# Kernel tuning notes

Hardware: AMD Instinct MI355X
Metric: run time of the kernel (lower is better)

## Reference

```python
import jax, jax.numpy as jnp
import numpy as np
from jax import lax

R = 2048          # proposals per image
K = 20            # foreground classes (VOC)
IMG_H, IMG_W = 800, 1333   # image_shape (height, width)
SCORE_THRESH = 0.5
NMS_THRESH = 0.5
TOPK = 100


def setup_inputs() -> dict:
    key = jax.random.key(0)
    k1, k2, k3 = jax.random.split(key, 3)
    # well-formed xyxy boxes roughly inside the image (some spill past edges to exercise clipping)
    xy = jax.random.uniform(k1, (R, 2)) * jnp.array([IMG_W * 0.9, IMG_H * 0.9], jnp.float32)
    wh = jax.random.uniform(k2, (R, 2)) * jnp.array([IMG_W * 0.3, IMG_H * 0.3], jnp.float32) + 4.0
    boxes = jnp.concatenate([xy, xy + wh], axis=1).astype(jnp.float32)          # [R,4]
    scores = jax.random.uniform(k3, (R, K + 1), dtype=jnp.float32)              # [R,K+1]
    return {"boxes": boxes, "scores": scores}


def _pairwise_iou(b):
    # b: [R,4] xyxy -> [R,R] IoU
    area = (b[:, 2] - b[:, 0]) * (b[:, 3] - b[:, 1])
    lt = jnp.maximum(b[:, None, :2], b[None, :, :2])
    rb = jnp.minimum(b[:, None, 2:], b[None, :, 2:])
    wh = jnp.clip(rb - lt, 0.0)
    inter = wh[..., 0] * wh[..., 1]
    union = area[:, None] + area[None, :] - inter
    return inter / jnp.maximum(union, 1e-9)


def _nms_single_class(scores_c, valid_c, boxes):
    # Greedy NMS over one class; padded candidates carry valid=False and never
    # get kept nor suppress anything (matches torchvision nms semantics).
    order = jnp.argsort(-scores_c)                      # descending by score
    iou = _pairwise_iou(boxes[order])                   # [R,R]
    v = valid_c[order]
    idx = jnp.arange(R)

    def body(i, keep):
        suppressed = jnp.any(keep & (iou[i] > NMS_THRESH) & (idx < i))
        return keep.at[i].set(v[i] & ~suppressed)

    keep_sorted = lax.fori_loop(0, R, body, jnp.zeros((R,), bool))
    return jnp.zeros((R,), bool).at[order].set(keep_sorted)


def reference(boxes, scores):
    scores_fg = scores[:, :-1]                                            # drop background col -> [R,K]
    finite = jnp.all(jnp.isfinite(boxes), axis=1) & jnp.all(jnp.isfinite(scores), axis=1)
    # Boxes.clip(image_shape): x in [0,W], y in [0,H]
    bx = jnp.stack([jnp.clip(boxes[:, 0], 0.0, IMG_W),
                    jnp.clip(boxes[:, 1], 0.0, IMG_H),
                    jnp.clip(boxes[:, 2], 0.0, IMG_W),
                    jnp.clip(boxes[:, 3], 0.0, IMG_H)], axis=1)           # [R,4]
    filt = (scores_fg > SCORE_THRESH) & finite[:, None]                    # [R,K]
    # batched_nms: independent greedy NMS per class (vmapped over classes)
    keep = jax.vmap(_nms_single_class, in_axes=(1, 1, None))(scores_fg, filt, bx)  # [K,R]
    masked = jnp.where(keep, scores_fg.T, -jnp.inf).reshape(-1)            # [K*R]
    top_s, top_i = lax.top_k(masked, TOPK)                                 # global topk (= keep[:topk])
    pred_classes = top_i // R
    pred_inds = top_i % R
    top_b = bx[pred_inds]                                                  # [TOPK,4]
    return top_s, top_b, pred_classes, pred_inds
```

## Files before the change

### kernel.cpp

```cpp
#include <hip/hip_runtime.h>
#include <hip/hip_bf16.h>
#include <math.h>

#define R 2048
#define K 20
#define TOPK 100
#define SCORE_TH 0.5f
#define NMS_TH 0.5f
#define IMGW 1333.0f
#define IMGH 800.0f

typedef unsigned long long u64;
typedef unsigned int u32;

#define MAPF_MINF 0x007FFFFFu
#define MAPF_TH 0xBF000000u

__device__ __forceinline__ u32 mapf(float f) {
  u32 b = __float_as_uint(f);
  return (b & 0x80000000u) ? ~b : (b | 0x80000000u);
}
__device__ __forceinline__ float unmapf(u32 u) {
  u32 b = (u & 0x80000000u) ? (u & 0x7FFFFFFFu) : ~u;
  return __uint_as_float(b);
}

__global__ void prep_kernel(const float* __restrict__ boxes,
                            const float* __restrict__ scores,
                            float* __restrict__ bx,
                            int* __restrict__ finite) {
  int r = blockIdx.x * blockDim.x + threadIdx.x;
  if (r >= R) return;
  float x1 = boxes[r * 4 + 0], y1 = boxes[r * 4 + 1];
  float x2 = boxes[r * 4 + 2], y2 = boxes[r * 4 + 3];
  bool fin = isfinite(x1) && isfinite(y1) && isfinite(x2) && isfinite(y2);
  for (int c = 0; c < K + 1; ++c) fin = fin && isfinite(scores[r * (K + 1) + c]);
  bx[r * 4 + 0] = fminf(fmaxf(x1, 0.0f), IMGW);
  bx[r * 4 + 1] = fminf(fmaxf(y1, 0.0f), IMGH);
  bx[r * 4 + 2] = fminf(fmaxf(x2, 0.0f), IMGW);
  bx[r * 4 + 3] = fminf(fmaxf(y2, 0.0f), IMGH);
  finite[r] = fin ? 1 : 0;
}

__global__ __launch_bounds__(1024) void sort_kernel(const float* __restrict__ scores,
                                                    const float* __restrict__ bx,
                                                    const int* __restrict__ finite,
                                                    u64* __restrict__ sortedkey,
                                                    float4* __restrict__ sboxs,
                                                    int* __restrict__ nvalid) {
  const int c = blockIdx.x;
  const int tid = threadIdx.x;
  __shared__ u64 sk[R];
  for (int r = tid; r < R; r += 1024) {
    float s = scores[r * (K + 1) + c];
    bool valid = (s > SCORE_TH) && (finite[r] != 0);
    u32 hi = valid ? mapf(s) : MAPF_MINF;
    sk[r] = ((u64)hi << 32) | (u32)(~(u32)r);
  }
  __syncthreads();
  for (int k = 2; k <= R; k <<= 1) {
    for (int j = k >> 1; j > 0; j >>= 1) {
      for (int i = tid; i < R; i += 1024) {
        int ixj = i ^ j;
        if (ixj > i) {
          u64 a = sk[i], b = sk[ixj];
          bool sw = ((i & k) == 0) ? (a < b) : (a > b);
          if (sw) { sk[i] = b; sk[ixj] = a; }
        }
      }
      __syncthreads();
    }
  }
  u64* skg = sortedkey + (size_t)c * R;
  float4* sbg = sboxs + (size_t)c * R;
  for (int i = tid; i < R; i += 1024) {
    u64 key = sk[i];
    skg[i] = key;
    u32 r = ~(u32)key;
    sbg[i] = reinterpret_cast<const float4*>(bx)[r];
    bool vi = ((u32)(key >> 32)) > MAPF_TH;
    if (i == 0 && !vi) nvalid[c] = 0;
    if (vi) {
      bool vlast = (i == R - 1);
      bool vn = vlast ? false : (((u32)(sk[i + 1] >> 32)) > MAPF_TH);
      if (vlast || !vn) nvalid[c] = i + 1;
    }
  }
}

__global__ __launch_bounds__(1024) void mask_kernel(const float4* __restrict__ sboxs,
                                                    const int* __restrict__ nvalid,
                                                    u64* __restrict__ maskbuf) {
  const int c = blockIdx.x;
  const int tid = threadIdx.x;
  const int lane = tid & 63;
  const int wave = tid >> 6;
  __shared__ float4 sb[R];
  __shared__ float sa[R];
  const float4* sbg = sboxs + (size_t)c * R;
  const int nv = nvalid[c];
  for (int i = tid; i < R; i += 1024) {
    float4 b = sbg[i];
    sb[i] = b;
    sa[i] = (b.z - b.x) * (b.w - b.y);
  }
  __syncthreads();
  const int wend = (nv + 63) >> 6;
  u64* mrowbase = maskbuf + (size_t)c * R * 32;
  for (int row = blockIdx.y * 16 + wave; row < nv; row += 128) {
    float4 b = sb[row];
    float ai = sa[row];
    u64 myword = 0;
    int wstart = row >> 6;
    for (int w = wstart; w < wend; ++w) {
      int col = (w << 6) + lane;
      float4 q = sb[col];
      float lx = fmaxf(b.x, q.x), ly = fmaxf(b.y, q.y);
      float rx = fminf(b.z, q.z), ry = fminf(b.w, q.w);
      float ww = fmaxf(rx - lx, 0.0f), hh = fmaxf(ry - ly, 0.0f);
      float inter = ww * hh;
      float uni = ai + sa[col] - inter;
      bool bit = (col > row) && (inter / fmaxf(uni, 1e-9f) > NMS_TH);
      u64 word = __ballot(bit);
      if (lane == w) myword = word;
    }
    u64* mrow = mrowbase + (size_t)row * 32;
    if (lane < 32) mrow[lane] = myword;
  }
}

__global__ __launch_bounds__(64) void scan_kernel(const u64* __restrict__ sortedkey,
                                                  const int* __restrict__ nvalid,
                                                  const u64* __restrict__ maskbuf,
                                                  u64* __restrict__ keybuf) {
  const int c = blockIdx.x;
  const int lane = threadIdx.x;
  const int nv = nvalid[c];
  const u64* mb = maskbuf + (size_t)c * R * 32;
  u64 remv = 0, keepm = 0;
  u64 ring[16];
#pragma unroll
  for (int s = 0; s < 16; ++s)
    ring[s] = (s < nv && lane < 32) ? mb[(size_t)s * 32 + lane] : 0ULL;
  for (int ib = 0; ib < nv; ib += 16) {
#pragma unroll
    for (int s = 0; s < 16; ++s) {
      int i = ib + s;
      bool act = i < nv;
      int widx = i >> 6;
      int bit = i & 63;
      u64 wv = __shfl(remv, widx, 64);
      bool keep = act && !((wv >> bit) & 1ULL);
      if (keep) {
        remv |= ring[s];
        if (lane == widx) keepm |= (1ULL << bit);
      }
      int ipf = i + 16;
      ring[s] = (ipf < nv && lane < 32) ? mb[(size_t)ipf * 32 + lane] : 0ULL;
    }
  }
  __shared__ u64 kw[32];
  if (lane < 32) kw[lane] = keepm;
  __syncthreads();
  const u64* skg = sortedkey + (size_t)c * R;
  for (int i = lane; i < R; i += 64) {
    u64 key = skg[i];
    bool kept = (i < nv) && ((kw[i >> 6] >> (i & 63)) & 1ULL);
    u32 r = ~(u32)key;
    u32 flat = (u32)c * R + r;
    u32 hi = kept ? (u32)(key >> 32) : MAPF_MINF;
    keybuf[flat] = ((u64)hi << 32) | (u32)(~flat);
  }
}

__global__ __launch_bounds__(64) void nms_kernel(const float* __restrict__ scores,
                                                 const float* __restrict__ bx,
                                                 const int* __restrict__ finite,
                                                 u64* __restrict__ keybuf) {
  const int c = blockIdx.x;
  const int lane = threadIdx.x;
  __shared__ u64 skeys[R];
  __shared__ float4 sbox[R];
  __shared__ float sarea[R];
  __shared__ unsigned short kidx[R];
  __shared__ unsigned char keepr[R];
  for (int r = lane; r < R; r += 64) {
    float s = scores[r * (K + 1) + c];
    bool valid = (s > SCORE_TH) && (finite[r] != 0);
    float sv = valid ? s : -INFINITY;
    skeys[r] = ((u64)mapf(sv) << 32) | (u32)(~(u32)r);
    keepr[r] = 0;
  }
  __syncthreads();
  for (int k = 2; k <= R; k <<= 1) {
    for (int j = k >> 1; j > 0; j >>= 1) {
      for (int i = lane; i < R; i += 64) {
        int ixj = i ^ j;
        if (ixj > i) {
          u64 a = skeys[i], b = skeys[ixj];
          bool sw = ((i & k) == 0) ? (a < b) : (a > b);
          if (sw) { skeys[i] = b; skeys[ixj] = a; }
        }
      }
      __syncthreads();
    }
  }
  for (int i = lane; i < R; i += 64) {
    int r = (int)(~(u32)skeys[i]);
    const float4 b = reinterpret_cast<const float4*>(bx)[r];
    sbox[i] = b;
    sarea[i] = (b.z - b.x) * (b.w - b.y);
  }
  __syncthreads();
  int m = 0;
  for (int i = 0; i < R; ++i) {
    u64 key = skeys[i];
    float s = unmapf((u32)(key >> 32));
    if (!(s > SCORE_TH)) break;
    int r = (int)(~(u32)key);
    float4 b = sbox[i];
    float ai = sarea[i];
    bool sup = false;
    for (int j = lane; j < m; j += 64) {
      int jj = kidx[j];
      float4 kb = sbox[jj];
      float lx = fmaxf(b.x, kb.x), ly = fmaxf(b.y, kb.y);
      float rx = fminf(b.z, kb.z), ry = fminf(b.w, kb.w);
      float w = fmaxf(rx - lx, 0.0f), h = fmaxf(ry - ly, 0.0f);
      float inter = w * h;
      float uni = ai + sarea[jj] - inter;
      if (inter / fmaxf(uni, 1e-9f) > NMS_TH) sup = true;
    }
    bool kept = !__any(sup);
    if (kept) {
      if (lane == 0) { kidx[m] = (unsigned short)i; keepr[r] = 1; }
      __syncthreads();
      m++;
    }
  }
  __syncthreads();
  for (int r = lane; r < R; r += 64) {
    float s = scores[r * (K + 1) + c];
    u32 flat = (u32)(c * R + r);
    float sv = keepr[r] ? s : -INFINITY;
    keybuf[flat] = ((u64)mapf(sv) << 32) | (u32)(~flat);
  }
}

__global__ __launch_bounds__(1024) void chunk_kernel(const u64* __restrict__ in,
                                                     int nin,
                                                     u64* __restrict__ outk) {
  const int t = blockIdx.x;
  const int tid = threadIdx.x;
  __shared__ u64 s[1024];
  int gi = t * 1024 + tid;
  s[tid] = (gi < nin) ? in[gi] : 0ULL;
  __syncthreads();
  for (int k = 2; k <= 1024; k <<= 1) {
    for (int j = k >> 1; j > 0; j >>= 1) {
      int ixj = tid ^ j;
      if (ixj > tid) {
        u64 a = s[tid], b = s[ixj];
        bool sw = ((tid & k) == 0) ? (a < b) : (a > b);
        if (sw) { s[tid] = b; s[ixj] = a; }
      }
      __syncthreads();
    }
  }
  if (tid < 128) outk[t * 128 + tid] = s[tid];
}

__global__ __launch_bounds__(1024) void final_kernel(const u64* __restrict__ cand,
                                                     int nin,
                                                     const float* __restrict__ bx,
                                                     float* __restrict__ out) {
  const int tid = threadIdx.x;
  __shared__ u64 s[1024];
  s[tid] = (tid < nin) ? cand[tid] : 0ULL;
  __syncthreads();
  for (int k = 2; k <= 1024; k <<= 1) {
    for (int j = k >> 1; j > 0; j >>= 1) {
      int ixj = tid ^ j;
      if (ixj > tid) {
        u64 a = s[tid], b = s[ixj];
        bool sw = ((tid & k) == 0) ? (a < b) : (a > b);
        if (sw) { s[tid] = b; s[ixj] = a; }
      }
      __syncthreads();
    }
  }
  if (tid < TOPK) {
    u64 key = s[tid];
    float sc = unmapf((u32)(key >> 32));
    u32 flat = ~(u32)key;
    int c = (int)(flat >> 11);
    int r = (int)(flat & 2047);
    out[tid] = sc;
    out[100 + 4 * tid + 0] = bx[r * 4 + 0];
    out[100 + 4 * tid + 1] = bx[r * 4 + 1];
    out[100 + 4 * tid + 2] = bx[r * 4 + 2];
    out[100 + 4 * tid + 3] = bx[r * 4 + 3];
    out[500 + tid] = (float)c;
    out[600 + tid] = (float)r;
  }
}

extern "C" void kernel_launch(void* const* d_in, const int* in_sizes, int n_in,
                              void* d_out, int out_size, void* d_ws, size_t ws_size,
                              hipStream_t stream) {
  const float* boxes = (const float*)d_in[0];
  const float* scores = (const float*)d_in[1];
  float* out = (float*)d_out;
  char* ws = (char*)d_ws;
  float* bx = (float*)(ws + 0);
  int* finite = (int*)(ws + 32768);
  (void)in_sizes; (void)n_in; (void)out_size;

  prep_kernel<<<8, 256, 0, stream>>>(boxes, scores, bx, finite);

  if (ws_size >= 11908096) {
    u64* sortedkey = (u64*)(ws + 40960);
    float4* sboxs = (float4*)(ws + 368640);
    int* nvalid = (int*)(ws + 1024000);
    u64* maskbuf = (u64*)(ws + 1048576);
    u64* keybuf = (u64*)(ws + 11534336);
    u64* cand1 = (u64*)(ws + 11862016);
    u64* cand2 = (u64*)(ws + 11902976);
    sort_kernel<<<K, 1024, 0, stream>>>(scores, bx, finite, sortedkey, sboxs, nvalid);
    mask_kernel<<<dim3(K, 8), 1024, 0, stream>>>(sboxs, nvalid, maskbuf);
    scan_kernel<<<K, 64, 0, stream>>>(sortedkey, nvalid, maskbuf, keybuf);
    chunk_kernel<<<40, 1024, 0, stream>>>(keybuf, K * R, cand1);
    chunk_kernel<<<5, 1024, 0, stream>>>(cand1, 5120, cand2);
    final_kernel<<<1, 1024, 0, stream>>>(cand2, 640, bx, out);
  } else {
    u64* keybuf = (u64*)(ws + 40960);
    u64* cand1 = (u64*)(ws + 368640);
    u64* cand2 = (u64*)(ws + 409600);
    nms_kernel<<<K, 64, 0, stream>>>(scores, bx, finite, keybuf);
    chunk_kernel<<<40, 1024, 0, stream>>>(keybuf, K * R, cand1);
    chunk_kernel<<<5, 1024, 0, stream>>>(cand1, 5120, cand2);
    final_kernel<<<1, 1024, 0, stream>>>(cand2, 640, bx, out);
  }
}
```

Measured before the change: 257.2 us.

## Fuse prep into sort, stage mask rows in LDS, emit per-class top-128 candidates

Folds the box clipping and finiteness check into the per-class sort kernel, which removes the prep launch and its intermediate buffers. The scan kernel now double-buffers 64-row mask windows in shared memory and compacts kept detections into at most 128 candidates per class plus a keep bitmap. A single final kernel sorts the 2560 candidates and fills any tail slots with -inf entries, replacing two chunk-sort launches. The fallback nms path is dropped, and each class sort now rereads all score columns per row to test finiteness.

```diff
diff --git a/kernel.cpp b/kernel.cpp
--- a/kernel.cpp
+++ b/kernel.cpp
@@ -24,36 +24,35 @@
   u32 b = (u & 0x80000000u) ? (u & 0x7FFFFFFFu) : ~u;
   return __uint_as_float(b);
 }
-
-__global__ void prep_kernel(const float* __restrict__ boxes,
-                            const float* __restrict__ scores,
-                            float* __restrict__ bx,
-                            int* __restrict__ finite) {
-  int r = blockIdx.x * blockDim.x + threadIdx.x;
-  if (r >= R) return;
-  float x1 = boxes[r * 4 + 0], y1 = boxes[r * 4 + 1];
-  float x2 = boxes[r * 4 + 2], y2 = boxes[r * 4 + 3];
-  bool fin = isfinite(x1) && isfinite(y1) && isfinite(x2) && isfinite(y2);
-  for (int c = 0; c < K + 1; ++c) fin = fin && isfinite(scores[r * (K + 1) + c]);
-  bx[r * 4 + 0] = fminf(fmaxf(x1, 0.0f), IMGW);
-  bx[r * 4 + 1] = fminf(fmaxf(y1, 0.0f), IMGH);
-  bx[r * 4 + 2] = fminf(fmaxf(x2, 0.0f), IMGW);
-  bx[r * 4 + 3] = fminf(fmaxf(y2, 0.0f), IMGH);
-  finite[r] = fin ? 1 : 0;
+__device__ __forceinline__ float4 clipbox(float4 b) {
+  float4 o;
+  o.x = fminf(fmaxf(b.x, 0.0f), IMGW);
+  o.y = fminf(fmaxf(b.y, 0.0f), IMGH);
+  o.z = fminf(fmaxf(b.z, 0.0f), IMGW);
+  o.w = fminf(fmaxf(b.w, 0.0f), IMGH);
+  return o;
 }
 
 __global__ __launch_bounds__(1024) void sort_kernel(const float* __restrict__ scores,
-                                                    const float* __restrict__ bx,
-                                                    const int* __restrict__ finite,
+                                                    const float* __restrict__ boxes,
                                                     u64* __restrict__ sortedkey,
                                                     float4* __restrict__ sboxs,
                                                     int* __restrict__ nvalid) {
   const int c = blockIdx.x;
   const int tid = threadIdx.x;
   __shared__ u64 sk[R];
+  __shared__ float4 cb[R];
   for (int r = tid; r < R; r += 1024) {
-    float s = scores[r * (K + 1) + c];
-    bool valid = (s > SCORE_TH) && (finite[r] != 0);
+    float4 b = reinterpret_cast<const float4*>(boxes)[r];
+    bool fin = isfinite(b.x) && isfinite(b.y) && isfinite(b.z) && isfinite(b.w);
+    float s = 0.0f;
+    for (int c2 = 0; c2 < K + 1; ++c2) {
+      float v = scores[r * (K + 1) + c2];
+      fin = fin && isfinite(v);
+      if (c2 == c) s = v;
+    }
+    cb[r] = clipbox(b);
+    bool valid = (s > SCORE_TH) && fin;
     u32 hi = valid ? mapf(s) : MAPF_MINF;
     sk[r] = ((u64)hi << 32) | (u32)(~(u32)r);
   }
@@ -76,8 +75,8 @@
   for (int i = tid; i < R; i += 1024) {
     u64 key = sk[i];
     skg[i] = key;
-    u32 r = ~(u32)key;
-    sbg[i] = reinterpret_cast<const float4*>(bx)[r];
+    u32 r = (~(u32)key) & 2047u;
+    sbg[i] = cb[r];
     bool vi = ((u32)(key >> 32)) > MAPF_TH;
     if (i == 0 && !vi) nvalid[c] = 0;
     if (vi) {
@@ -132,176 +131,156 @@
 __global__ __launch_bounds__(64) void scan_kernel(const u64* __restrict__ sortedkey,
                                                   const int* __restrict__ nvalid,
                                                   const u64* __restrict__ maskbuf,
-                                                  u64* __restrict__ keybuf) {
+                                                  u64* __restrict__ cand,
+                                                  int* __restrict__ nkept,
+                                                  u32* __restrict__ keepbm) {
   const int c = blockIdx.x;
   const int lane = threadIdx.x;
   const int nv = nvalid[c];
   const u64* mb = maskbuf + (size_t)c * R * 32;
+  const u64* skg = sortedkey + (size_t)c * R;
+  __shared__ u64 win[2][2048];
+  __shared__ u64 keepw[32];
+  __shared__ int pref[32];
+  __shared__ u64 lcand[128];
+  __shared__ u32 bm[64];
+  if (lane < 32) keepw[lane] = 0;
+  bm[lane] = 0;
+  lcand[lane] = 0;
+  lcand[lane + 64] = 0;
+
+  const int ngroups = (nv + 63) >> 6;
+  if (ngroups > 0) {
+    int lim = (nv < 64 ? nv : 64) * 32;
+    for (int t = lane; t < 2048; t += 64) win[0][t] = (t < lim) ? mb[t] : 0;
+  }
+  __syncthreads();
+
   u64 remv = 0, keepm = 0;
-  u64 ring[16];
-#pragma unroll
-  for (int s = 0; s < 16; ++s)
-    ring[s] = (s < nv && lane < 32) ? mb[(size_t)s * 32 + lane] : 0ULL;
-  for (int ib = 0; ib < nv; ib += 16) {
-#pragma unroll
-    for (int s = 0; s < 16; ++s) {
-      int i = ib + s;
-      bool act = i < nv;
-      int widx = i >> 6;
-      int bit = i & 63;
-      u64 wv = __shfl(remv, widx, 64);
-      bool keep = act && !((wv >> bit) & 1ULL);
+  for (int g = 0; g < ngroups; ++g) {
+    const int buf = g & 1;
+    if (g + 1 < ngroups) {
+      int base = (g + 1) << 6;
+      int nrows = nv - base; if (nrows > 64) nrows = 64;
+      int lim = nrows * 32;
+      for (int t = lane; t < 2048; t += 64)
+        win[buf ^ 1][t] = (t < lim) ? mb[(size_t)base * 32 + t] : 0;
+    }
+    const int rb = g << 6;
+    int rend = nv - rb; if (rend > 64) rend = 64;
+    for (int b = 0; b < rend; ++b) {
+      u64 wv = __shfl(remv, g, 64);
+      bool keep = !((wv >> b) & 1ull);
       if (keep) {
-        remv |= ring[s];
-        if (lane == widx) keepm |= (1ULL << bit);
+        u64 v = (lane < 32) ? win[buf][b * 32 + lane] : 0;
+        remv |= v;
+        if (lane == g) keepm |= (1ull << b);
       }
-      int ipf = i + 16;
-      ring[s] = (ipf < nv && lane < 32) ? mb[(size_t)ipf * 32 + lane] : 0ULL;
-    }
-  }
-  __shared__ u64 kw[32];
-  if (lane < 32) kw[lane] = keepm;
-  __syncthreads();
-  const u64* skg = sortedkey + (size_t)c * R;
-  for (int i = lane; i < R; i += 64) {
-    u64 key = skg[i];
-    bool kept = (i < nv) && ((kw[i >> 6] >> (i & 63)) & 1ULL);
-    u32 r = ~(u32)key;
-    u32 flat = (u32)c * R + r;
-    u32 hi = kept ? (u32)(key >> 32) : MAPF_MINF;
-    keybuf[flat] = ((u64)hi << 32) | (u32)(~flat);
-  }
-}
-
-__global__ __launch_bounds__(64) void nms_kernel(const float* __restrict__ scores,
-                                                 const float* __restrict__ bx,
-                                                 const int* __restrict__ finite,
-                                                 u64* __restrict__ keybuf) {
-  const int c = blockIdx.x;
-  const int lane = threadIdx.x;
-  __shared__ u64 skeys[R];
-  __shared__ float4 sbox[R];
-  __shared__ float sarea[R];
-  __shared__ unsigned short kidx[R];
-  __shared__ unsigned char keepr[R];
-  for (int r = lane; r < R; r += 64) {
-    float s = scores[r * (K + 1) + c];
-    bool valid = (s > SCORE_TH) && (finite[r] != 0);
-    float sv = valid ? s : -INFINITY;
-    skeys[r] = ((u64)mapf(sv) << 32) | (u32)(~(u32)r);
-    keepr[r] = 0;
-  }
-  __syncthreads();
-  for (int k = 2; k <= R; k <<= 1) {
+    }
+    __syncthreads();
+  }
+  if (lane < 32) keepw[lane] = keepm;
+  __syncthreads();
+  if (lane == 0) {
+    int run = 0;
+    for (int g = 0; g < ngroups; ++g) { pref[g] = run; run += (int)__popcll(keepw[g]); }
+    nkept[c] = run;
+  }
+  __syncthreads();
+  for (int g = 0; g < ngroups; ++g) {
+    u64 kw = keepw[g];
+    if ((kw >> lane) & 1ull) {
+      u64 below = lane ? (kw & ((1ull << lane) - 1ull)) : 0ull;
+      int slot = pref[g] + (int)__popcll(below);
+      u64 key = skg[(g << 6) + lane];
+      u32 r = (~(u32)key) & 2047u;
+      u32 flat = (u32)c * R + r;
+      atomicOr(&bm[r >> 5], 1u << (r & 31));
+      if (slot < 128) lcand[slot] = (key & 0xFFFFFFFF00000000ull) | (u64)(u32)(~flat);
+    }
+  }
+  __syncthreads();
+  cand[(size_t)c * 128 + lane] = lcand[lane];
+  cand[(size_t)c * 128 + 64 + lane] = lcand[lane + 64];
+  keepbm[c * 64 + lane] = bm[lane];
+}
+
+__global__ __launch_bounds__(1024) void final_kernel(const u64* __restrict__ cand,
+                                                     const int* __restrict__ nkept,
+                                                     const u32* __restrict__ keepbm,
+                                                     const float* __restrict__ boxes,
+                                                     float* __restrict__ out) {
+  const int tid = threadIdx.x;
+  __shared__ u64 s[4096];
+  __shared__ int nk_sh;
+  for (int i = tid; i < 4096; i += 1024) s[i] = (i < K * 128) ? cand[i] : 0ULL;
+  if (tid == 0) {
+    int nk = 0;
+    for (int c = 0; c < K; ++c) nk += nkept[c];
+    nk_sh = nk;
+  }
+  __syncthreads();
+  for (int k = 2; k <= 4096; k <<= 1) {
     for (int j = k >> 1; j > 0; j >>= 1) {
-      for (int i = lane; i < R; i += 64) {
+      for (int i = tid; i < 4096; i += 1024) {
         int ixj = i ^ j;
         if (ixj > i) {
-          u64 a = skeys[i], b = skeys[ixj];
+          u64 a = s[i], b = s[ixj];
           bool sw = ((i & k) == 0) ? (a < b) : (a > b);
-          if (sw) { skeys[i] = b; skeys[ixj] = a; }
+          if (sw) { s[i] = b; s[ixj] = a; }
         }
       }
       __syncthreads();
     }
   }
-  for (int i = lane; i < R; i += 64) {
-    int r = (int)(~(u32)skeys[i]);
-    const float4 b = reinterpret_cast<const float4*>(bx)[r];
-    sbox[i] = b;
-    sarea[i] = (b.z - b.x) * (b.w - b.y);
-  }
-  __syncthreads();
-  int m = 0;
-  for (int i = 0; i < R; ++i) {
-    u64 key = skeys[i];
-    float s = unmapf((u32)(key >> 32));
-    if (!(s > SCORE_TH)) break;
-    int r = (int)(~(u32)key);
-    float4 b = sbox[i];
-    float ai = sarea[i];
-    bool sup = false;
-    for (int j = lane; j < m; j += 64) {
-      int jj = kidx[j];
-      float4 kb = sbox[jj];
-      float lx = fmaxf(b.x, kb.x), ly = fmaxf(b.y, kb.y);
-      float rx = fminf(b.z, kb.z), ry = fminf(b.w, kb.w);
-      float w = fmaxf(rx - lx, 0.0f), h = fmaxf(ry - ly, 0.0f);
-      float inter = w * h;
-      float uni = ai + sarea[jj] - inter;
-      if (inter / fmaxf(uni, 1e-9f) > NMS_TH) sup = true;
-    }
-    bool kept = !__any(sup);
-    if (kept) {
-      if (lane == 0) { kidx[m] = (unsigned short)i; keepr[r] = 1; }
-      __syncthreads();
-      m++;
-    }
-  }
-  __syncthreads();
-  for (int r = lane; r < R; r += 64) {
-    float s = scores[r * (K + 1) + c];
-    u32 flat = (u32)(c * R + r);
-    float sv = keepr[r] ? s : -INFINITY;
-    keybuf[flat] = ((u64)mapf(sv) << 32) | (u32)(~flat);
-  }
-}
-
-__global__ __launch_bounds__(1024) void chunk_kernel(const u64* __restrict__ in,
-                                                     int nin,
-                                                     u64* __restrict__ outk) {
-  const int t = blockIdx.x;
-  const int tid = threadIdx.x;
-  __shared__ u64 s[1024];
-  int gi = t * 1024 + tid;
-  s[tid] = (gi < nin) ? in[gi] : 0ULL;
-  __syncthreads();
-  for (int k = 2; k <= 1024; k <<= 1) {
-    for (int j = k >> 1; j > 0; j >>= 1) {
-      int ixj = tid ^ j;
-      if (ixj > tid) {
-        u64 a = s[tid], b = s[ixj];
-        bool sw = ((tid & k) == 0) ? (a < b) : (a > b);
-        if (sw) { s[tid] = b; s[ixj] = a; }
+  const int nk = nk_sh;
+  if (nk >= TOPK) {
+    if (tid < TOPK) {
+      u64 key = s[tid];
+      u32 flat = ~(u32)key;
+      int c = (int)(flat >> 11);
+      int r = (int)(flat & 2047);
+      float4 b = clipbox(reinterpret_cast<const float4*>(boxes)[r]);
+      out[tid] = unmapf((u32)(key >> 32));
+      out[100 + 4 * tid + 0] = b.x;
+      out[100 + 4 * tid + 1] = b.y;
+      out[100 + 4 * tid + 2] = b.z;
+      out[100 + 4 * tid + 3] = b.w;
+      out[500 + tid] = (float)c;
+      out[600 + tid] = (float)r;
+    }
+  } else {
+    if (tid < nk) {
+      u64 key = s[tid];
+      u32 flat = ~(u32)key;
+      int c = (int)(flat >> 11);
+      int r = (int)(flat & 2047);
+      float4 b = clipbox(reinterpret_cast<const float4*>(boxes)[r]);
+      out[tid] = unmapf((u32)(key >> 32));
+      out[100 + 4 * tid + 0] = b.x;
+      out[100 + 4 * tid + 1] = b.y;
+      out[100 + 4 * tid + 2] = b.z;
+      out[100 + 4 * tid + 3] = b.w;
+      out[500 + tid] = (float)c;
+      out[600 + tid] = (float)r;
+    }
+    if (tid == 0) {
+      int w = nk;
+      for (u32 f = 0; f < (u32)(K * R) && w < TOPK; ++f) {
+        u32 cc = f >> 11, rr = f & 2047u;
+        if (!((keepbm[cc * 64 + (rr >> 5)] >> (rr & 31)) & 1u)) {
+          float4 b = clipbox(reinterpret_cast<const float4*>(boxes)[rr]);
+          out[w] = -INFINITY;
+          out[100 + 4 * w + 0] = b.x;
+          out[100 + 4 * w + 1] = b.y;
+          out[100 + 4 * w + 2] = b.z;
+          out[100 + 4 * w + 3] = b.w;
+          out[500 + w] = (float)cc;
+          out[600 + w] = (float)rr;
+          ++w;
+        }
       }
-      __syncthreads();
-    }
-  }
-  if (tid < 128) outk[t * 128 + tid] = s[tid];
-}
-
-__global__ __launch_bounds__(1024) void final_kernel(const u64* __restrict__ cand,
-                                                     int nin,
-                                                     const float* __restrict__ bx,
-                                                     float* __restrict__ out) {
-  const int tid = threadIdx.x;
-  __shared__ u64 s[1024];
-  s[tid] = (tid < nin) ? cand[tid] : 0ULL;
-  __syncthreads();
-  for (int k = 2; k <= 1024; k <<= 1) {
-    for (int j = k >> 1; j > 0; j >>= 1) {
-      int ixj = tid ^ j;
-      if (ixj > tid) {
-        u64 a = s[tid], b = s[ixj];
-        bool sw = ((tid & k) == 0) ? (a < b) : (a > b);
-        if (sw) { s[tid] = b; s[ixj] = a; }
-      }
-      __syncthreads();
-    }
-  }
-  if (tid < TOPK) {
-    u64 key = s[tid];
-    float sc = unmapf((u32)(key >> 32));
-    u32 flat = ~(u32)key;
-    int c = (int)(flat >> 11);
-    int r = (int)(flat & 2047);
-    out[tid] = sc;
-    out[100 + 4 * tid + 0] = bx[r * 4 + 0];
-    out[100 + 4 * tid + 1] = bx[r * 4 + 1];
-    out[100 + 4 * tid + 2] = bx[r * 4 + 2];
-    out[100 + 4 * tid + 3] = bx[r * 4 + 3];
-    out[500 + tid] = (float)c;
-    out[600 + tid] = (float)r;
+    }
   }
 }
 
@@ -312,33 +291,17 @@
   const float* scores = (const float*)d_in[1];
   float* out = (float*)d_out;
   char* ws = (char*)d_ws;
-  float* bx = (float*)(ws + 0);
-  int* finite = (int*)(ws + 32768);
-  (void)in_sizes; (void)n_in; (void)out_size;
-
-  prep_kernel<<<8, 256, 0, stream>>>(boxes, scores, bx, finite);
-
-  if (ws_size >= 11908096) {
-    u64* sortedkey = (u64*)(ws + 40960);
-    float4* sboxs = (float4*)(ws + 368640);
-    int* nvalid = (int*)(ws + 1024000);
-    u64* maskbuf = (u64*)(ws + 1048576);
-    u64* keybuf = (u64*)(ws + 11534336);
-    u64* cand1 = (u64*)(ws + 11862016);
-    u64* cand2 = (u64*)(ws + 11902976);
-    sort_kernel<<<K, 1024, 0, stream>>>(scores, bx, finite, sortedkey, sboxs, nvalid);
-    mask_kernel<<<dim3(K, 8), 1024, 0, stream>>>(sboxs, nvalid, maskbuf);
-    scan_kernel<<<K, 64, 0, stream>>>(sortedkey, nvalid, maskbuf, keybuf);
-    chunk_kernel<<<40, 1024, 0, stream>>>(keybuf, K * R, cand1);
-    chunk_kernel<<<5, 1024, 0, stream>>>(cand1, 5120, cand2);
-    final_kernel<<<1, 1024, 0, stream>>>(cand2, 640, bx, out);
-  } else {
-    u64* keybuf = (u64*)(ws + 40960);
-    u64* cand1 = (u64*)(ws + 368640);
-    u64* cand2 = (u64*)(ws + 409600);
-    nms_kernel<<<K, 64, 0, stream>>>(scores, bx, finite, keybuf);
-    chunk_kernel<<<40, 1024, 0, stream>>>(keybuf, K * R, cand1);
-    chunk_kernel<<<5, 1024, 0, stream>>>(cand1, 5120, cand2);
-    final_kernel<<<1, 1024, 0, stream>>>(cand2, 640, bx, out);
-  }
-}
+  u64* sortedkey = (u64*)(ws + 0);
+  float4* sboxs = (float4*)(ws + 327680);
+  int* nvalid = (int*)(ws + 983040);
+  u64* maskbuf = (u64*)(ws + 1048576);
+  u64* cand = (u64*)(ws + 11534336);
+  int* nkept = (int*)(ws + 11554816);
+  u32* keepbm = (u32*)(ws + 11555072);
+  (void)in_sizes; (void)n_in; (void)out_size; (void)ws_size;
+
+  sort_kernel<<<K, 1024, 0, stream>>>(scores, boxes, sortedkey, sboxs, nvalid);
+  mask_kernel<<<dim3(K, 8), 1024, 0, stream>>>(sboxs, nvalid, maskbuf);
+  scan_kernel<<<K, 64, 0, stream>>>(sortedkey, nvalid, maskbuf, cand, nkept, keepbm);
+  final_kernel<<<1, 1024, 0, stream>>>(cand, nkept, keepbm, boxes, out);
+}
```

Measured after the change: 414.9 us. +61.3%, slower.
